# Performance work log

Measured on AMD Instinct MI355X. Metric: run time of the kernel, lower is better.

Reference implementation:

```python
import jax, jax.numpy as jnp
import numpy as np

B, T, N, E = 8, 32, 128, 2048
IN_DIM, HID, OUT = 512, 512, 512
SLOPE = 0.2  # GATConv default negative_slope


def setup_inputs() -> dict:
    key = jax.random.key(0)
    ks = jax.random.split(key, 12)
    x = jax.random.normal(ks[0], (B, T, N, IN_DIM), jnp.float32)
    edge_index = jax.random.randint(ks[1], (B, T, 2, E), 0, N)
    valid_step_index = jax.random.randint(ks[2], (B,), 1, T + 1)
    def lin(k, o, i):
        return jax.random.normal(k, (o, i), jnp.float32) / np.sqrt(i).astype(np.float32)
    W1 = lin(ks[3], HID, IN_DIM)
    a1_src = jax.random.normal(ks[4], (HID,), jnp.float32) / np.sqrt(HID).astype(np.float32)
    a1_dst = jax.random.normal(ks[5], (HID,), jnp.float32) / np.sqrt(HID).astype(np.float32)
    b1 = jnp.zeros((HID,), jnp.float32)
    W2 = lin(ks[6], OUT, HID)
    a2_src = jax.random.normal(ks[7], (OUT,), jnp.float32) / np.sqrt(OUT).astype(np.float32)
    a2_dst = jax.random.normal(ks[8], (OUT,), jnp.float32) / np.sqrt(OUT).astype(np.float32)
    b2 = jnp.zeros((OUT,), jnp.float32)
    W_time = jax.random.normal(ks[9], (T, T), jnp.float32) / np.sqrt(T).astype(np.float32)
    b_time = jnp.zeros((T,), jnp.float32)
    return dict(x=x, edge_index=edge_index, valid_step_index=valid_step_index,
                W1=W1, a1_src=a1_src, a1_dst=a1_dst, b1=b1,
                W2=W2, a2_src=a2_src, a2_dst=a2_dst, b2=b2,
                W_time=W_time, b_time=b_time)


def _gat(x, src, dst, W, a_src, a_dst, b):
    # Single-head PyG GATConv (concat=True, heads=1), self-loops already appended.
    n = x.shape[0]
    h = x @ W.T                                             # [N, H]
    e = jax.nn.leaky_relu((h @ a_src)[src] + (h @ a_dst)[dst], SLOPE)  # [E]
    m = jax.ops.segment_max(e, dst, num_segments=n)
    m = jnp.where(jnp.isfinite(m), m, 0.0)
    p = jnp.exp(e - m[dst])
    denom = jax.ops.segment_sum(p, dst, num_segments=n)
    alpha = p / denom[dst]                                  # segment softmax over incoming edges
    return jax.ops.segment_sum(h[src] * alpha[:, None], dst, num_segments=n) + b


def reference(x, edge_index, valid_step_index, W1, a1_src, a1_dst, b1,
              W2, a2_src, a2_dst, b2, W_time, b_time):
    b_, t_, n_, _ = x.shape
    g = b_ * t_
    xf = x.reshape(g, n_, -1)
    ei = edge_index.reshape(g, 2, -1)
    # add self loops (PyG GATConv default add_self_loops=True)
    loops = jnp.broadcast_to(jnp.arange(n_)[None, None, :], (g, 2, n_))
    ei = jnp.concatenate([ei, loops], axis=-1)
    src, dst = ei[:, 0], ei[:, 1]
    gat = jax.vmap(_gat, in_axes=(0, 0, 0, None, None, None, None))
    h = jax.nn.gelu(gat(xf, src, dst, W1, a1_src, a1_dst, b1), approximate=False)
    # F.dropout(p=0.2) is identity in eval mode
    h = gat(h, src, dst, W2, a2_src, a2_dst, b2)
    y = h.reshape(b_, t_, n_, -1)
    mask = (jnp.arange(t_)[None, :] < valid_step_index[:, None]).astype(y.dtype)
    y = y * mask[:, :, None, None]
    # TemporalConv: Conv2d(T, T, 1) over time-as-channel = linear mix across time, then GELU, residual
    fused = jax.nn.gelu(jnp.einsum('ts,bsnf->btnf', W_time, y)
                        + b_time[None, :, None, None], approximate=False)
    return fused + y
```

## Files before the change

kernel.cpp:

```cpp
#include <hip/hip_runtime.h>

using u16 = unsigned short;
using u32 = unsigned int;

typedef __bf16 bf16x8 __attribute__((ext_vector_type(8)));
typedef float  f32x4  __attribute__((ext_vector_type(4)));

__device__ __forceinline__ u16 f2bf(float f) {
    u32 u = __float_as_uint(f);
    u32 r = u + 0x7fffu + ((u >> 16) & 1u);
    return (u16)(r >> 16);
}
__device__ __forceinline__ float bf2f(u16 u) {
    return __uint_as_float(((u32)u) << 16);
}
__device__ __forceinline__ float gelu_f(float x) {
    return 0.5f * x * (1.0f + erff(x * 0.70710678118654752440f));
}

#define GLOAD16(gp, lp) __builtin_amdgcn_global_load_lds( \
    (const __attribute__((address_space(1))) void*)(gp),  \
    (__attribute__((address_space(3))) void*)(lp), 16, 0, 0)
#define WAITV4  asm volatile("s_waitcnt vmcnt(4)" ::: "memory")
#define WAITV0  asm volatile("s_waitcnt vmcnt(0)" ::: "memory")
#define WAITL0  asm volatile("s_waitcnt lgkmcnt(0)" ::: "memory")

__global__ __launch_bounds__(256) void prep_kernel(
    const float* __restrict__ x, const float* __restrict__ W1, const float* __restrict__ W2,
    u16* __restrict__ Xb, u16* __restrict__ W1b, u16* __restrict__ W2b,
    float* __restrict__ Z)
{
    const int i0 = blockIdx.x * 256 + threadIdx.x;
    const int stride = gridDim.x * 256;
    if (i0 < 32768) ((float4*)Z)[i0] = make_float4(0.f, 0.f, 0.f, 0.f);
    for (int i = i0; i < 65536; i += stride) {
        float4 v = ((const float4*)W1)[i];
        ushort4 o; o.x = f2bf(v.x); o.y = f2bf(v.y); o.z = f2bf(v.z); o.w = f2bf(v.w);
        ((ushort4*)W1b)[i] = o;
    }
    for (int i = i0; i < 65536; i += stride) {
        float4 v = ((const float4*)W2)[i];
        ushort4 o; o.x = f2bf(v.x); o.y = f2bf(v.y); o.z = f2bf(v.z); o.w = f2bf(v.w);
        ((ushort4*)W2b)[i] = o;
    }
    for (int i = i0; i < 4194304; i += stride) {
        float4 v = ((const float4*)x)[i];
        ushort4 o; o.x = f2bf(v.x); o.y = f2bf(v.y); o.z = f2bf(v.z); o.w = f2bf(v.w);
        ((ushort4*)Xb)[i] = o;
    }
}

__global__ __launch_bounds__(256) void gat_gemm(
    const u16* __restrict__ A, const u16* __restrict__ Wb,
    const float* __restrict__ a_s, const float* __restrict__ a_d,
    u16* __restrict__ HT, float* __restrict__ SS, float* __restrict__ SD)
{
    __shared__ __align__(16) u16 SH[4][128 * 32];
    __shared__ float sA[128], dA[128];

    const int tid  = threadIdx.x;
    const int lane = tid & 63;
    const int w    = tid >> 6;
    const int wm   = w & 1, wn = w >> 1;
    const int fr   = lane & 15;
    const int grp  = lane >> 4;
    const int bid  = (blockIdx.x & 7) * 128 + (blockIdx.x >> 3);
    const int g    = bid >> 2;
    const int tn   = (bid & 3) * 128;

    if (tid < 128) { sA[tid] = 0.f; dA[tid] = 0.f; }

    const int l3 = lane >> 3, l7 = lane & 7;
    const int cs = l7 ^ l3;
    const u16* Ag0 = A  + (size_t)g * 65536
                   + (size_t)(w * 32 + 2 * l3 + (cs >> 2)) * 512 + (cs & 3) * 8;
    const u16* Bg0 = Wb + (size_t)(tn + w * 32 + 2 * l3 + (cs >> 2)) * 512 + (cs & 3) * 8;

    const int sw = ((((fr & 1) << 2) | grp) ^ ((fr >> 1) & 7)) * 8;

    f32x4 acc[4][4] = {};

    GLOAD16(Ag0,                 &SH[0][w * 1024]);
    GLOAD16(Ag0 + 16 * 512,      &SH[0][w * 1024 + 512]);
    GLOAD16(Bg0,                 &SH[2][w * 1024]);
    GLOAD16(Bg0 + 16 * 512,      &SH[2][w * 1024 + 512]);
    GLOAD16(Ag0 + 32,            &SH[1][w * 1024]);
    GLOAD16(Ag0 + 16 * 512 + 32, &SH[1][w * 1024 + 512]);
    GLOAD16(Bg0 + 32,            &SH[3][w * 1024]);
    GLOAD16(Bg0 + 16 * 512 + 32, &SH[3][w * 1024 + 512]);

    for (int kt = 0; kt < 16; ++kt) {
        const int cur = kt & 1;
        if (kt < 15) { WAITV4; } else { WAITV0; }
        __builtin_amdgcn_s_barrier();
        bf16x8 af[4], bf[4];
        #pragma unroll
        for (int i = 0; i < 4; ++i) {
            af[i] = *(const bf16x8*)&SH[cur][(wm * 32 + i * 8 + (fr >> 1)) * 64 + sw];
            bf[i] = *(const bf16x8*)&SH[2 + cur][(wn * 32 + i * 8 + (fr >> 1)) * 64 + sw];
        }
        WAITL0;
        __builtin_amdgcn_sched_barrier(0);
        __builtin_amdgcn_s_barrier();
        if (kt < 14) {
            GLOAD16(Ag0 + (kt + 2) * 32,            &SH[cur][w * 1024]);
            GLOAD16(Ag0 + 16 * 512 + (kt + 2) * 32, &SH[cur][w * 1024 + 512]);
            GLOAD16(Bg0 + (kt + 2) * 32,            &SH[2 + cur][w * 1024]);
            GLOAD16(Bg0 + 16 * 512 + (kt + 2) * 32, &SH[2 + cur][w * 1024 + 512]);
        }
        #pragma unroll
        for (int i = 0; i < 4; ++i)
            #pragma unroll
            for (int j = 0; j < 4; ++j)
                acc[i][j] = __builtin_amdgcn_mfma_f32_16x16x32_bf16(af[i], bf[j], acc[i][j], 0, 0, 0);
    }

    u16* Hs = &SH[0][0];

    #pragma unroll
    for (int i = 0; i < 4; ++i) {
        int node0 = wm * 64 + i * 16 + grp * 4;
        int c = node0 >> 3, in8 = node0 & 7;
        #pragma unroll
        for (int j = 0; j < 4; ++j) {
            int fl = wn * 64 + j * 16 + fr;
            ushort4 o;
            o.x = f2bf(acc[i][j][0]); o.y = f2bf(acc[i][j][1]);
            o.z = f2bf(acc[i][j][2]); o.w = f2bf(acc[i][j][3]);
            *(ushort4*)&Hs[fl * 128 + ((c ^ fr) * 8) + in8] = o;
        }
    }

    float asv[4], adv[4];
    #pragma unroll
    for (int j = 0; j < 4; ++j) {
        int f = tn + wn * 64 + j * 16 + fr;
        asv[j] = a_s[f]; adv[j] = a_d[f];
    }
    #pragma unroll
    for (int i = 0; i < 4; ++i) {
        int node0 = wm * 64 + i * 16 + grp * 4;
        #pragma unroll
        for (int r = 0; r < 4; ++r) {
            float s = acc[i][0][r] * asv[0] + acc[i][1][r] * asv[1]
                    + acc[i][2][r] * asv[2] + acc[i][3][r] * asv[3];
            float d = acc[i][0][r] * adv[0] + acc[i][1][r] * adv[1]
                    + acc[i][2][r] * adv[2] + acc[i][3][r] * adv[3];
            #pragma unroll
            for (int off = 1; off < 16; off <<= 1) {
                s += __shfl_xor(s, off);
                d += __shfl_xor(d, off);
            }
            if (fr == 0) {
                atomicAdd(&sA[node0 + r], s);
                atomicAdd(&dA[node0 + r], d);
            }
        }
    }
    __syncthreads();

    u16* Hg = HT + (size_t)g * 65536;
    #pragma unroll
    for (int it = 0; it < 8; ++it) {
        int fl  = it * 16 + (tid >> 4);
        int blk = tid & 15;
        uint4 v = *(const uint4*)&Hs[fl * 128 + ((blk ^ (fl & 15)) * 8)];
        *(uint4*)&Hg[(size_t)(tn + fl) * 128 + blk * 8] = v;
    }
    if (tid < 128) {
        atomicAdd(&SS[g * 128 + tid], sA[tid]);
        atomicAdd(&SD[g * 128 + tid], dA[tid]);
    }
}

template<int MODE>
__global__ __launch_bounds__(512) void gat_agg(
    const u16* __restrict__ HT, const int* __restrict__ ei,
    const float* __restrict__ SS, const float* __restrict__ SD,
    const float* __restrict__ bias, const int* __restrict__ valid,
    u16* __restrict__ outU)
{
    __shared__ u16 Hts[32768];
    __shared__ u32 cntw[2048];
    __shared__ float stf[512];

    const int tid  = threadIdx.x;
    const int lane = tid & 63;
    const int w    = tid >> 6;
    const int rl   = lane & 15;
    const int grp  = lane >> 4;
    const int q    = blockIdx.x;
    const int g    = (q & 7) * 32 + (q >> 4);
    const int hf   = (q >> 3) & 1;
    const int bb   = g >> 5, tt = g & 31;

    const int4* es = (const int4*)(ei + (size_t)g * 4096);
    int4 e0 = es[tid], e1 = es[512 + tid];

    const u16* Hg = HT + (size_t)g * 65536 + (size_t)hf * 256 * 128;
    #pragma unroll
    for (int it = 0; it < 8; ++it) {
        int fl = it * 32 + (tid >> 4);
        int blk = tid & 15;
        GLOAD16(Hg + (size_t)fl * 128 + ((blk ^ (fl & 15)) * 8), &Hts[it * 4096 + w * 512]);
    }

    for (int i = tid; i < 2048; i += 512) cntw[i] = 0u;
    if (tid < 128) {
        stf[tid]       = SS[g * 128 + tid];
        stf[128 + tid] = SD[g * 128 + tid];
    }
    __syncthreads();

    atomicAdd(&cntw[e1.x * 16 + (e0.x >> 3)], 1u << ((e0.x & 7) * 4));
    atomicAdd(&cntw[e1.y * 16 + (e0.y >> 3)], 1u << ((e0.y & 7) * 4));
    atomicAdd(&cntw[e1.z * 16 + (e0.z >> 3)], 1u << ((e0.z & 7) * 4));
    atomicAdd(&cntw[e1.w * 16 + (e0.w >> 3)], 1u << ((e0.w & 7) * 4));
    if (tid < 128) atomicAdd(&cntw[tid * 16 + (tid >> 3)], 1u << ((tid & 7) * 4));
    __syncthreads();

    for (int r = 0; r < 16; ++r) {
        int m = w * 16 + r;
        float sdm = stf[128 + m];
        u32 w0 = cntw[m * 16 + (lane >> 3)];
        u32 w1 = cntw[m * 16 + 8 + (lane >> 3)];
        u32 c0 = (w0 >> ((lane & 7) * 4)) & 15u;
        u32 c1 = (w1 >> ((lane & 7) * 4)) & 15u;
        float E0 = stf[lane] + sdm;      E0 = E0 > 0.f ? E0 : 0.2f * E0;
        float E1 = stf[lane + 64] + sdm; E1 = E1 > 0.f ? E1 : 0.2f * E1;
        float mx = fmaxf(c0 ? E0 : -1e30f, c1 ? E1 : -1e30f);
        #pragma unroll
        for (int off = 1; off < 64; off <<= 1) mx = fmaxf(mx, __shfl_xor(mx, off));
        float p = (c0 ? (float)c0 * __expf(E0 - mx) : 0.f)
                + (c1 ? (float)c1 * __expf(E1 - mx) : 0.f);
        #pragma unroll
        for (int off = 1; off < 64; off <<= 1) p += __shfl_xor(p, off);
        if (lane == 0) { stf[256 + m] = mx; stf[384 + m] = 1.f / p; }
    }
    __syncthreads();

    const int m = w * 16 + rl;
    const float sdm = stf[128 + m], Mm = stf[256 + m], rDm = stf[384 + m];
    bf16x8 pa[4];
    #pragma unroll
    for (int kb = 0; kb < 4; ++kb) {
        u32 word = cntw[m * 16 + kb * 4 + grp];
        #pragma unroll
        for (int e = 0; e < 8; ++e) {
            u32 c = (word >> (e * 4)) & 15u;
            int s = kb * 32 + grp * 8 + e;
            float ev = stf[s] + sdm; ev = ev > 0.f ? ev : 0.2f * ev;
            float p = c ? (float)c * __expf(ev - Mm) * rDm : 0.f;
            pa[kb][e] = (__bf16)p;
        }
    }

    const float msk = (MODE == 1) ? ((tt < valid[bb]) ? 1.f : 0.f) : 1.f;
    #pragma unroll 1
    for (int jc = 0; jc < 4; ++jc) {
        f32x4 acc2[4] = {};
        __builtin_amdgcn_s_setprio(1);
        #pragma unroll
        for (int j4 = 0; j4 < 4; ++j4) {
            int fl = jc * 64 + j4 * 16 + rl;
            #pragma unroll
            for (int kb = 0; kb < 4; ++kb) {
                bf16x8 hb = *(const bf16x8*)&Hts[fl * 128 + (((kb * 4 + grp) ^ (fl & 15)) * 8)];
                acc2[j4] = __builtin_amdgcn_mfma_f32_16x16x32_bf16(pa[kb], hb, acc2[j4], 0, 0, 0);
            }
        }
        __builtin_amdgcn_s_setprio(0);
        #pragma unroll
        for (int j4 = 0; j4 < 4; ++j4) {
            int f = hf * 256 + jc * 64 + j4 * 16 + rl;
            float bv = bias[f];
            #pragma unroll
            for (int r = 0; r < 4; ++r) {
                int m2 = w * 16 + grp * 4 + r;
                if (MODE == 0)
                    outU[(size_t)g * 65536 + m2 * 512 + f] = f2bf(gelu_f(acc2[j4][r] + bv));
                else
                    outU[(size_t)g * 65536 + m2 * 512 + f] = f2bf((acc2[j4][r] + bv) * msk);
            }
        }
    }
}

__global__ __launch_bounds__(256) void timemix_kernel(const u16* __restrict__ yb,
                                                      float* __restrict__ out,
                                                      const float* __restrict__ Wt,
                                                      const float* __restrict__ bt) {
    __shared__ float wsm[1024];
    __shared__ float bts[32];
    int tid = threadIdx.x;
    for (int i = tid; i < 1024; i += 256) wsm[i] = Wt[i];
    if (tid < 32) bts[tid] = bt[tid];
    __syncthreads();
    int blk = blockIdx.x;
    int b = blk >> 8;
    int rem = blk & 255;
    int n = rem >> 1;
    int f = (rem & 1) * 256 + tid;
    size_t base = ((size_t)b * 4096 + n) * 512 + f;
    float ys[32];
    #pragma unroll
    for (int s = 0; s < 32; ++s) ys[s] = bf2f(yb[base + (size_t)s * 65536]);
    #pragma unroll
    for (int t = 0; t < 32; ++t) {
        float a = bts[t];
        #pragma unroll
        for (int s = 0; s < 32; ++s) a += wsm[t * 32 + s] * ys[s];
        out[base + (size_t)t * 65536] = gelu_f(a) + ys[t];
    }
}

extern "C" void kernel_launch(void* const* d_in, const int* in_sizes, int n_in,
                              void* d_out, int out_size, void* d_ws, size_t ws_size,
                              hipStream_t stream) {
    const float* x     = (const float*)d_in[0];
    const int*   ei    = (const int*)d_in[1];
    const int*   valid = (const int*)d_in[2];
    const float* W1    = (const float*)d_in[3];
    const float* a1s   = (const float*)d_in[4];
    const float* a1d   = (const float*)d_in[5];
    const float* b1    = (const float*)d_in[6];
    const float* W2    = (const float*)d_in[7];
    const float* a2s   = (const float*)d_in[8];
    const float* a2d   = (const float*)d_in[9];
    const float* b2    = (const float*)d_in[10];
    const float* Wt    = (const float*)d_in[11];
    const float* bt    = (const float*)d_in[12];
    float* out = (float*)d_out;

    char* ws = (char*)d_ws;
    u16* Xb    = (u16*)(ws);
    u16* HTb   = (u16*)(ws + 33554432);
    u16* W1b   = (u16*)(ws + 67108864);
    u16* W2b   = (u16*)(ws + 67633152);
    float* SS1 = (float*)(ws + 68157440);
    float* SD1 = (float*)(ws + 68288512);
    float* SS2 = (float*)(ws + 68419584);
    float* SD2 = (float*)(ws + 68550656);

    prep_kernel<<<2048, 256, 0, stream>>>(x, W1, W2, Xb, W1b, W2b, SS1);

    gat_gemm<<<1024, 256, 0, stream>>>(Xb, W1b, a1s, a1d, HTb, SS1, SD1);
    gat_agg<0><<<512, 512, 0, stream>>>(HTb, ei, SS1, SD1, b1, nullptr, Xb);

    gat_gemm<<<1024, 256, 0, stream>>>(Xb, W2b, a2s, a2d, HTb, SS2, SD2);
    gat_agg<1><<<512, 512, 0, stream>>>(HTb, ei, SS2, SD2, b2, valid, Xb);

    timemix_kernel<<<2048, 256, 0, stream>>>(Xb, out, Wt, bt);
}
```

Before: 176.4 us.

## Split edge counting and softmax stats into separate per-graph kernel

```diff
diff --git a/kernel.cpp b/kernel.cpp
--- a/kernel.cpp
+++ b/kernel.cpp
@@ -173,10 +173,63 @@
     }
 }
 
+__global__ __launch_bounds__(256) void stats_kernel(
+    const int* __restrict__ ei, const float* __restrict__ SS, const float* __restrict__ SD,
+    u32* __restrict__ CNT, float* __restrict__ STF)
+{
+    __shared__ u32 cntw[2048];
+    __shared__ float stf[512];
+    const int tid = threadIdx.x, lane = tid & 63, w = tid >> 6;
+    const int q = blockIdx.x;
+    const int g = (q & 7) * 32 + (q >> 3);
+
+    for (int i = tid; i < 2048; i += 256) cntw[i] = 0u;
+    if (tid < 128) {
+        stf[tid]       = SS[g * 128 + tid];
+        stf[128 + tid] = SD[g * 128 + tid];
+    }
+    __syncthreads();
+
+    const int4* es = (const int4*)(ei + (size_t)g * 4096);
+    for (int i = tid; i < 512; i += 256) {
+        int4 s4 = es[i], d4 = es[512 + i];
+        atomicAdd(&cntw[d4.x * 16 + (s4.x >> 3)], 1u << ((s4.x & 7) * 4));
+        atomicAdd(&cntw[d4.y * 16 + (s4.y >> 3)], 1u << ((s4.y & 7) * 4));
+        atomicAdd(&cntw[d4.z * 16 + (s4.z >> 3)], 1u << ((s4.z & 7) * 4));
+        atomicAdd(&cntw[d4.w * 16 + (s4.w >> 3)], 1u << ((s4.w & 7) * 4));
+    }
+    if (tid < 128) atomicAdd(&cntw[tid * 16 + (tid >> 3)], 1u << ((tid & 7) * 4));
+    __syncthreads();
+
+    for (int r = 0; r < 32; ++r) {
+        int m = w * 32 + r;
+        float sdm = stf[128 + m];
+        u32 w0 = cntw[m * 16 + (lane >> 3)];
+        u32 w1 = cntw[m * 16 + 8 + (lane >> 3)];
+        u32 c0 = (w0 >> ((lane & 7) * 4)) & 15u;
+        u32 c1 = (w1 >> ((lane & 7) * 4)) & 15u;
+        float E0 = stf[lane] + sdm;      E0 = E0 > 0.f ? E0 : 0.2f * E0;
+        float E1 = stf[lane + 64] + sdm; E1 = E1 > 0.f ? E1 : 0.2f * E1;
+        float mx = fmaxf(c0 ? E0 : -1e30f, c1 ? E1 : -1e30f);
+        #pragma unroll
+        for (int off = 1; off < 64; off <<= 1) mx = fmaxf(mx, __shfl_xor(mx, off));
+        float p = (c0 ? (float)c0 * __expf(E0 - mx) : 0.f)
+                + (c1 ? (float)c1 * __expf(E1 - mx) : 0.f);
+        #pragma unroll
+        for (int off = 1; off < 64; off <<= 1) p += __shfl_xor(p, off);
+        if (lane == 0) { stf[256 + m] = mx; stf[384 + m] = 1.f / p; }
+    }
+    __syncthreads();
+
+    uint4* co = (uint4*)(CNT + (size_t)g * 2048);
+    const uint4* ci = (const uint4*)cntw;
+    for (int i = tid; i < 512; i += 256) co[i] = ci[i];
+    if (tid < 128) ((float4*)(STF + (size_t)g * 512))[tid] = ((const float4*)stf)[tid];
+}
+
 template<int MODE>
 __global__ __launch_bounds__(512) void gat_agg(
-    const u16* __restrict__ HT, const int* __restrict__ ei,
-    const float* __restrict__ SS, const float* __restrict__ SD,
+    const u16* __restrict__ HT, const u32* __restrict__ CNT, const float* __restrict__ STF,
     const float* __restrict__ bias, const int* __restrict__ valid,
     u16* __restrict__ outU)
 {
@@ -194,9 +247,6 @@
     const int hf   = (q >> 3) & 1;
     const int bb   = g >> 5, tt = g & 31;
 
-    const int4* es = (const int4*)(ei + (size_t)g * 4096);
-    int4 e0 = es[tid], e1 = es[512 + tid];
-
     const u16* Hg = HT + (size_t)g * 65536 + (size_t)hf * 256 * 128;
     #pragma unroll
     for (int it = 0; it < 8; ++it) {
@@ -204,39 +254,9 @@
         int blk = tid & 15;
         GLOAD16(Hg + (size_t)fl * 128 + ((blk ^ (fl & 15)) * 8), &Hts[it * 4096 + w * 512]);
     }
-
-    for (int i = tid; i < 2048; i += 512) cntw[i] = 0u;
-    if (tid < 128) {
-        stf[tid]       = SS[g * 128 + tid];
-        stf[128 + tid] = SD[g * 128 + tid];
-    }
-    __syncthreads();
-
-    atomicAdd(&cntw[e1.x * 16 + (e0.x >> 3)], 1u << ((e0.x & 7) * 4));
-    atomicAdd(&cntw[e1.y * 16 + (e0.y >> 3)], 1u << ((e0.y & 7) * 4));
-    atomicAdd(&cntw[e1.z * 16 + (e0.z >> 3)], 1u << ((e0.z & 7) * 4));
-    atomicAdd(&cntw[e1.w * 16 + (e0.w >> 3)], 1u << ((e0.w & 7) * 4));
-    if (tid < 128) atomicAdd(&cntw[tid * 16 + (tid >> 3)], 1u << ((tid & 7) * 4));
-    __syncthreads();
-
-    for (int r = 0; r < 16; ++r) {
-        int m = w * 16 + r;
-        float sdm = stf[128 + m];
-        u32 w0 = cntw[m * 16 + (lane >> 3)];
-        u32 w1 = cntw[m * 16 + 8 + (lane >> 3)];
-        u32 c0 = (w0 >> ((lane & 7) * 4)) & 15u;
-        u32 c1 = (w1 >> ((lane & 7) * 4)) & 15u;
-        float E0 = stf[lane] + sdm;      E0 = E0 > 0.f ? E0 : 0.2f * E0;
-        float E1 = stf[lane + 64] + sdm; E1 = E1 > 0.f ? E1 : 0.2f * E1;
-        float mx = fmaxf(c0 ? E0 : -1e30f, c1 ? E1 : -1e30f);
-        #pragma unroll
-        for (int off = 1; off < 64; off <<= 1) mx = fmaxf(mx, __shfl_xor(mx, off));
-        float p = (c0 ? (float)c0 * __expf(E0 - mx) : 0.f)
-                + (c1 ? (float)c1 * __expf(E1 - mx) : 0.f);
-        #pragma unroll
-        for (int off = 1; off < 64; off <<= 1) p += __shfl_xor(p, off);
-        if (lane == 0) { stf[256 + m] = mx; stf[384 + m] = 1.f / p; }
-    }
+    GLOAD16(CNT + (size_t)g * 2048 + w * 256 + lane * 4, &cntw[w * 256]);
+    if (w < 2)
+        GLOAD16(STF + (size_t)g * 512 + w * 256 + lane * 4, &stf[w * 256]);
     __syncthreads();
 
     const int m = w * 16 + rl;
@@ -341,14 +361,18 @@
     float* SD1 = (float*)(ws + 68288512);
     float* SS2 = (float*)(ws + 68419584);
     float* SD2 = (float*)(ws + 68550656);
+    u32*   CNT = (u32*)(ws + 68681728);
+    float* STF = (float*)(ws + 70778880);
 
     prep_kernel<<<2048, 256, 0, stream>>>(x, W1, W2, Xb, W1b, W2b, SS1);
 
     gat_gemm<<<1024, 256, 0, stream>>>(Xb, W1b, a1s, a1d, HTb, SS1, SD1);
-    gat_agg<0><<<512, 512, 0, stream>>>(HTb, ei, SS1, SD1, b1, nullptr, Xb);
+    stats_kernel<<<256, 256, 0, stream>>>(ei, SS1, SD1, CNT, STF);
+    gat_agg<0><<<512, 512, 0, stream>>>(HTb, CNT, STF, b1, nullptr, Xb);
 
     gat_gemm<<<1024, 256, 0, stream>>>(Xb, W2b, a2s, a2d, HTb, SS2, SD2);
-    gat_agg<1><<<512, 512, 0, stream>>>(HTb, ei, SS2, SD2, b2, valid, Xb);
+    stats_kernel<<<256, 256, 0, stream>>>(ei, SS2, SD2, CNT, STF);
+    gat_agg<1><<<512, 512, 0, stream>>>(HTb, CNT, STF, b2, valid, Xb);
 
     timemix_kernel<<<2048, 256, 0, stream>>>(Xb, out, Wt, bt);
 }
```

Measured after the change: 197.3 us. +11.9%, slower.
